# Kernel optimization log

Hardware: AMD Instinct MI355X
Metric: run time of the kernel (lower is better)

## Reference

```python
import jax, jax.numpy as jnp
import numpy as np

THRESHOLD = 2.0 / 3.0


def _quantize_1_58_bit(weight):
    """BitNet b1.58: ternary {-1,0,+1} * scale, scale = mean(|w|) clamped."""
    scale = jnp.clip(jnp.mean(jnp.abs(weight)), 1e-5, 1000.0)
    weight_norm = jnp.clip(weight / scale, -10.0, 10.0)
    q = jnp.where(weight_norm > THRESHOLD, 1.0,
                  jnp.where(weight_norm < -THRESHOLD, -1.0, 0.0)).astype(weight.dtype)
    return q, scale


def setup_inputs() -> dict:
    key = jax.random.key(0)
    k1, k2 = jax.random.split(key)
    B, S, D_IN, D_OUT = 4, 2048, 4096, 4096
    x = jax.random.normal(k1, (B, S, D_IN), dtype=jnp.float32)
    weight = jax.random.normal(k2, (D_OUT, D_IN), dtype=jnp.float32)
    bias = jnp.zeros((D_OUT,), dtype=jnp.float32)
    return {"x": x, "weight": weight, "bias": bias}


def reference(x, weight, bias):
    # Training-path forward value == eval-path forward value:
    # dequantized ternary weight, F.linear semantics (x @ W.T + b).
    q, scale = _quantize_1_58_bit(weight)
    weight_q = q * scale  # [out, in]
    out = jnp.einsum('bsi,oi->bso', x, weight_q) + bias
    return out
```

## Files before the change

kernel.cpp:

```cpp
#include <hip/hip_runtime.h>
#include <hip/hip_bf16.h>
#include <stdint.h>


typedef __bf16 bf16x8 __attribute__((ext_vector_type(8)));
typedef float f32x4 __attribute__((ext_vector_type(4)));
typedef unsigned short u16x8 __attribute__((ext_vector_type(8)));

__device__ __forceinline__ unsigned short f2bf_rne(float f) {
  union { float f; unsigned int u; } v; v.f = f;
  unsigned int u = v.u;
  u += 0x7FFFu + ((u >> 16) & 1u);
  return (unsigned short)(u >> 16);
}

__global__ void absum_kernel(const float4* __restrict__ w, int n4,
                             double* __restrict__ out) {
  float s = 0.f;
  for (int i = blockIdx.x * blockDim.x + threadIdx.x; i < n4;
       i += gridDim.x * blockDim.x) {
    float4 v = w[i];
    s += fabsf(v.x) + fabsf(v.y) + fabsf(v.z) + fabsf(v.w);
  }
#pragma unroll
  for (int off = 32; off > 0; off >>= 1) s += __shfl_down(s, off);
  __shared__ float partial[4];
  if ((threadIdx.x & 63) == 0) partial[threadIdx.x >> 6] = s;
  __syncthreads();
  if (threadIdx.x == 0)
    atomicAdd(out, (double)(partial[0] + partial[1] + partial[2] + partial[3]));
}

__global__ void quant_kernel(const float4* __restrict__ w, int n8,
                             const double* __restrict__ sum, double inv_cnt,
                             u16x8* __restrict__ q) {
  float scale = (float)fmin(fmax(sum[0] * inv_cnt, 1e-5), 1000.0);
  const float T = 2.0f / 3.0f;
  for (int i = blockIdx.x * blockDim.x + threadIdx.x; i < n8;
       i += gridDim.x * blockDim.x) {
    float4 a = w[2 * i], b = w[2 * i + 1];
    float f[8] = {a.x, a.y, a.z, a.w, b.x, b.y, b.z, b.w};
    u16x8 o;
#pragma unroll
    for (int j = 0; j < 8; ++j) {
      float n = f[j] / scale;
      o[j] = (n > T) ? 0x3F80u : ((n < -T) ? 0xBF80u : 0u);
    }
    q[i] = o;
  }
}

__global__ void xcvt_kernel(const float4* __restrict__ x, int n8,
                            u16x8* __restrict__ xb) {
  for (int i = blockIdx.x * blockDim.x + threadIdx.x; i < n8;
       i += gridDim.x * blockDim.x) {
    float4 a = x[2 * i], b = x[2 * i + 1];
    float f[8] = {a.x, a.y, a.z, a.w, b.x, b.y, b.z, b.w};
    u16x8 o;
#pragma unroll
    for (int j = 0; j < 8; ++j) o[j] = f2bf_rne(f[j]);
    xb[i] = o;
  }
}


#define BKT 64

#define FENCE() asm volatile("" ::: "memory")
#define BAR() __builtin_amdgcn_s_barrier()
#define WAIT_LGKM0() asm volatile("s_waitcnt lgkmcnt(0)" ::: "memory")
#define WAIT_VM8() asm volatile("s_waitcnt vmcnt(8)" ::: "memory")

__global__ __launch_bounds__(512, 2)
void gemm_kernel(const ushort* __restrict__ xb,
                 const ushort* __restrict__ qb,
                 const float* __restrict__ bias,
                 const double* __restrict__ sum,
                 float* __restrict__ out,
                 int M, int N, int K, double inv_cnt) {
  __shared__ __align__(16) ushort As[2][2][128][64];
  __shared__ __align__(16) ushort Bs[2][2][128][64];

  const int t = threadIdx.x;
  const int w = t >> 6;
  const int lane = t & 63;
  const int wm = w >> 2;
  const int wn = w & 3;
  const int lm = lane & 15;
  const int lk = lane >> 4;

  const int nbx = N >> 8;
  const int cpx = gridDim.x >> 3;
  const int id = blockIdx.x;
  const int swz = (id & 7) * cpx + (id >> 3);
  const int bx = swz % nbx;
  const int by = swz / nbx;
  const int m0 = by << 8;
  const int n0 = bx << 8;

  const int srow = lane >> 3;
  const int schunk = (lane & 7) ^ srow;
  const ushort* aSrc = xb + (size_t)(m0 + w * 8 + srow) * K + schunk * 8;
  const ushort* bSrc = qb + (size_t)(n0 + w * 8 + srow) * K + schunk * 8;

#define STAGE_A(BUF, H, KT)                                                    \
  do {                                                                         \
    _Pragma("unroll") for (int s_ = 0; s_ < 2; ++s_) {                         \
      __builtin_amdgcn_global_load_lds(                                        \
          (const __attribute__((address_space(1))) void*)(                     \
              aSrc + (size_t)((H) * 128 + s_ * 64) * K + (KT) * BKT),          \
          (__attribute__((address_space(3))) void*)(                           \
              &As[BUF][H][s_ * 64 + w * 8][0]),                                \
          16, 0, 0);                                                           \
    }                                                                          \
  } while (0)

#define STAGE_B(BUF, H, KT)                                                    \
  do {                                                                         \
    _Pragma("unroll") for (int s_ = 0; s_ < 2; ++s_) {                         \
      __builtin_amdgcn_global_load_lds(                                        \
          (const __attribute__((address_space(1))) void*)(                     \
              bSrc + (size_t)((H) * 128 + s_ * 64) * K + (KT) * BKT),          \
          (__attribute__((address_space(3))) void*)(                           \
              &Bs[BUF][H][s_ * 64 + w * 8][0]),                                \
          16, 0, 0);                                                           \
    }                                                                          \
  } while (0)

#define RD_A(BUF, MH)                                                          \
  _Pragma("unroll") for (int mq = 0; mq < 4; ++mq)                             \
  _Pragma("unroll") for (int ks = 0; ks < 2; ++ks)                             \
      af[mq][ks] = *(const bf16x8*)&As[BUF][wm][(MH) * 64 + mq * 16 + lm]      \
                                      [((ks * 4 + lk) ^ (lm & 7)) * 8];

#define RD_B(BUF, NF0)                                                         \
  _Pragma("unroll") for (int nf = (NF0); nf < (NF0) + 2; ++nf)                 \
  _Pragma("unroll") for (int ks = 0; ks < 2; ++ks)                             \
      bf[nf][ks] =                                                             \
          *(const bf16x8*)&Bs[BUF][wn >> 1][(wn & 1) * 64 + nf * 16 + lm]      \
                              [((ks * 4 + lk) ^ (lm & 7)) * 8];

#define MFMA_Q(MH, NB)                                                         \
  _Pragma("unroll") for (int mq = 0; mq < 4; ++mq)                             \
  _Pragma("unroll") for (int nq = 0; nq < 2; ++nq)                             \
  _Pragma("unroll") for (int ks = 0; ks < 2; ++ks)                             \
      acc[(MH) * 4 + mq][(NB) + nq] =                                          \
          __builtin_amdgcn_mfma_f32_16x16x32_bf16(                             \
              af[mq][ks], bf[(NB) + nq][ks], acc[(MH) * 4 + mq][(NB) + nq],    \
              0, 0, 0);

  f32x4 acc[8][4] = {};
  bf16x8 af[4][2];
  bf16x8 bf[4][2];

  STAGE_A(0, 0, 0); STAGE_A(0, 1, 0);
  STAGE_B(0, 0, 0); STAGE_B(0, 1, 0);
  STAGE_B(1, 0, 1); STAGE_B(1, 1, 1);
  STAGE_A(1, 0, 1); STAGE_A(1, 1, 1);
  WAIT_VM8();
  FENCE(); BAR(); FENCE();

  const int NT = K / BKT;
  for (int i = 0; i < NT / 2; ++i) {
    const int kt2 = (2 * i + 2 < NT) ? (2 * i + 2) : (NT - 1);
    const int kt3 = (2 * i + 3 < NT) ? (2 * i + 3) : (NT - 1);

    RD_A(0, 0); RD_B(0, 0);
    FENCE(); BAR(); WAIT_LGKM0();
    __builtin_amdgcn_s_setprio(1); MFMA_Q(0, 0); __builtin_amdgcn_s_setprio(0);
    FENCE(); BAR();

    RD_B(0, 2);
    FENCE(); BAR(); WAIT_LGKM0();
    __builtin_amdgcn_s_setprio(1); MFMA_Q(0, 2); __builtin_amdgcn_s_setprio(0);
    FENCE(); BAR();

    RD_A(0, 1);
    STAGE_B(0, 0, kt2); STAGE_B(0, 1, kt2);
    FENCE(); BAR(); WAIT_LGKM0();
    __builtin_amdgcn_s_setprio(1); MFMA_Q(1, 2); __builtin_amdgcn_s_setprio(0);
    FENCE(); BAR();

    STAGE_A(0, 0, kt2); STAGE_A(0, 1, kt2);
    FENCE(); BAR();
    __builtin_amdgcn_s_setprio(1); MFMA_Q(1, 0); __builtin_amdgcn_s_setprio(0);
    WAIT_VM8();
    FENCE(); BAR();

    RD_A(1, 0); RD_B(1, 0);
    FENCE(); BAR(); WAIT_LGKM0();
    __builtin_amdgcn_s_setprio(1); MFMA_Q(0, 0); __builtin_amdgcn_s_setprio(0);
    FENCE(); BAR();

    RD_B(1, 2);
    FENCE(); BAR(); WAIT_LGKM0();
    __builtin_amdgcn_s_setprio(1); MFMA_Q(0, 2); __builtin_amdgcn_s_setprio(0);
    FENCE(); BAR();

    RD_A(1, 1);
    STAGE_B(1, 0, kt3); STAGE_B(1, 1, kt3);
    FENCE(); BAR(); WAIT_LGKM0();
    __builtin_amdgcn_s_setprio(1); MFMA_Q(1, 2); __builtin_amdgcn_s_setprio(0);
    FENCE(); BAR();

    STAGE_A(1, 0, kt3); STAGE_A(1, 1, kt3);
    FENCE(); BAR();
    __builtin_amdgcn_s_setprio(1); MFMA_Q(1, 0); __builtin_amdgcn_s_setprio(0);
    WAIT_VM8();
    FENCE(); BAR();
  }

  float scale = (float)fmin(fmax(sum[0] * inv_cnt, 1e-5), 1000.0);

#pragma unroll
  for (int nf = 0; nf < 4; ++nf) {
    const int col = n0 + wn * 64 + nf * 16 + lm;
    const float bv = bias[col];
#pragma unroll
    for (int mf = 0; mf < 8; ++mf) {
      const int row = m0 + wm * 128 + mf * 16 + lk * 4;
      float* op = out + (size_t)row * N + col;
#pragma unroll
      for (int r = 0; r < 4; ++r)
        op[(size_t)r * N] = acc[mf][nf][r] * scale + bv;
    }
  }
}

extern "C" void kernel_launch(void* const* d_in, const int* in_sizes, int n_in,
                              void* d_out, int out_size, void* d_ws,
                              size_t ws_size, hipStream_t stream) {
  const float* x = (const float*)d_in[0];
  const float* w = (const float*)d_in[1];
  const float* bias = (const float*)d_in[2];
  float* out = (float*)d_out;

  const int DOUT = in_sizes[2];
  const int DIN = in_sizes[1] / DOUT;
  const int M = in_sizes[0] / DIN;
  const int N = DOUT, K = DIN;

  char* ws = (char*)d_ws;
  double* sum = (double*)ws;
  ushort* xb = (ushort*)(ws + 256);
  ushort* qb = (ushort*)(ws + 256 + (size_t)M * K * 2);

  const double inv_cnt = 1.0 / ((double)N * (double)K);

  hipMemsetAsync(d_ws, 0, 8, stream);

  const int wn4 = (N * K) / 4;
  const int wn8 = (N * K) / 8;
  absum_kernel<<<1024, 256, 0, stream>>>((const float4*)w, wn4, sum);
  quant_kernel<<<4096, 256, 0, stream>>>((const float4*)w, wn8, sum, inv_cnt,
                                         (u16x8*)qb);
  const int xn8 = (M * K) / 8;
  xcvt_kernel<<<8192, 256, 0, stream>>>((const float4*)x, xn8, (u16x8*)xb);

  const int nwg = (M >> 8) * (N >> 8);
  gemm_kernel<<<dim3(nwg), 512, 0, stream>>>(xb, qb, bias, sum, out, M, N, K,
                                             inv_cnt);
}
```

Baseline: 587.1 us.

## Replace double-buffered 256x256 GEMM with single-buffered 256x128 tiles and two-stage absum

The GEMM drops its hand-scheduled double-buffered pipeline with interleaved barriers, waitcnts and prefetch. It now uses 256x128 tiles, 256 threads, a single LDS buffer and a plain load, syncthreads, compute, syncthreads loop. The weight abs-sum reduction changes from a double atomicAdd after a memset to per-block partials plus a one-block final reduction, which removes the memset. Without overlap of global loads and MFMA, the GEMM is likely to stall on memory latency, though the smaller tiles and LDS footprint allow more resident workgroups per CU.

```diff
diff --git a/kernel.cpp b/kernel.cpp
--- a/kernel.cpp
+++ b/kernel.cpp
@@ -14,8 +14,8 @@
   return (unsigned short)(u >> 16);
 }
 
-__global__ void absum_kernel(const float4* __restrict__ w, int n4,
-                             double* __restrict__ out) {
+__global__ void absum_part(const float4* __restrict__ w, int n4,
+                           float* __restrict__ partial) {
   float s = 0.f;
   for (int i = blockIdx.x * blockDim.x + threadIdx.x; i < n4;
        i += gridDim.x * blockDim.x) {
@@ -24,11 +24,23 @@
   }
 #pragma unroll
   for (int off = 32; off > 0; off >>= 1) s += __shfl_down(s, off);
-  __shared__ float partial[4];
-  if ((threadIdx.x & 63) == 0) partial[threadIdx.x >> 6] = s;
+  __shared__ float lds[4];
+  if ((threadIdx.x & 63) == 0) lds[threadIdx.x >> 6] = s;
   __syncthreads();
   if (threadIdx.x == 0)
-    atomicAdd(out, (double)(partial[0] + partial[1] + partial[2] + partial[3]));
+    partial[blockIdx.x] = lds[0] + lds[1] + lds[2] + lds[3];
+}
+
+__global__ void absum_final(const float* __restrict__ partial, int n,
+                            double* __restrict__ out) {
+  double s = 0.0;
+  for (int i = threadIdx.x; i < n; i += blockDim.x) s += (double)partial[i];
+#pragma unroll
+  for (int off = 32; off > 0; off >>= 1) s += __shfl_down(s, off);
+  __shared__ double lds[4];
+  if ((threadIdx.x & 63) == 0) lds[threadIdx.x >> 6] = s;
+  __syncthreads();
+  if (threadIdx.x == 0) out[0] = lds[0] + lds[1] + lds[2] + lds[3];
 }
 
 __global__ void quant_kernel(const float4* __restrict__ w, int n8,
@@ -66,79 +78,49 @@
 
 #define BKT 64
 
-#define FENCE() asm volatile("" ::: "memory")
-#define BAR() __builtin_amdgcn_s_barrier()
-#define WAIT_LGKM0() asm volatile("s_waitcnt lgkmcnt(0)" ::: "memory")
-#define WAIT_VM8() asm volatile("s_waitcnt vmcnt(8)" ::: "memory")
-
-__global__ __launch_bounds__(512, 2)
+__global__ __launch_bounds__(256, 2)
 void gemm_kernel(const ushort* __restrict__ xb,
                  const ushort* __restrict__ qb,
                  const float* __restrict__ bias,
                  const double* __restrict__ sum,
                  float* __restrict__ out,
                  int M, int N, int K, double inv_cnt) {
-  __shared__ __align__(16) ushort As[2][2][128][64];
-  __shared__ __align__(16) ushort Bs[2][2][128][64];
+  __shared__ __align__(16) ushort As[256][64];
+  __shared__ __align__(16) ushort Bs[128][64];
 
   const int t = threadIdx.x;
   const int w = t >> 6;
   const int lane = t & 63;
-  const int wm = w >> 2;
-  const int wn = w & 3;
+  const int wm = w >> 1;
+  const int wn = w & 1;
   const int lm = lane & 15;
   const int lk = lane >> 4;
 
-  const int nbx = N >> 8;
+  const int nbx = N >> 7;
   const int cpx = gridDim.x >> 3;
   const int id = blockIdx.x;
   const int swz = (id & 7) * cpx + (id >> 3);
   const int bx = swz % nbx;
   const int by = swz / nbx;
   const int m0 = by << 8;
-  const int n0 = bx << 8;
+  const int n0 = bx << 7;
 
   const int srow = lane >> 3;
   const int schunk = (lane & 7) ^ srow;
   const ushort* aSrc = xb + (size_t)(m0 + w * 8 + srow) * K + schunk * 8;
   const ushort* bSrc = qb + (size_t)(n0 + w * 8 + srow) * K + schunk * 8;
 
-#define STAGE_A(BUF, H, KT)                                                    \
-  do {                                                                         \
-    _Pragma("unroll") for (int s_ = 0; s_ < 2; ++s_) {                         \
-      __builtin_amdgcn_global_load_lds(                                        \
-          (const __attribute__((address_space(1))) void*)(                     \
-              aSrc + (size_t)((H) * 128 + s_ * 64) * K + (KT) * BKT),          \
-          (__attribute__((address_space(3))) void*)(                           \
-              &As[BUF][H][s_ * 64 + w * 8][0]),                                \
-          16, 0, 0);                                                           \
-    }                                                                          \
-  } while (0)
-
-#define STAGE_B(BUF, H, KT)                                                    \
-  do {                                                                         \
-    _Pragma("unroll") for (int s_ = 0; s_ < 2; ++s_) {                         \
-      __builtin_amdgcn_global_load_lds(                                        \
-          (const __attribute__((address_space(1))) void*)(                     \
-              bSrc + (size_t)((H) * 128 + s_ * 64) * K + (KT) * BKT),          \
-          (__attribute__((address_space(3))) void*)(                           \
-              &Bs[BUF][H][s_ * 64 + w * 8][0]),                                \
-          16, 0, 0);                                                           \
-    }                                                                          \
-  } while (0)
-
-#define RD_A(BUF, MH)                                                          \
+#define RD_A(MH)                                                               \
   _Pragma("unroll") for (int mq = 0; mq < 4; ++mq)                             \
   _Pragma("unroll") for (int ks = 0; ks < 2; ++ks)                             \
-      af[mq][ks] = *(const bf16x8*)&As[BUF][wm][(MH) * 64 + mq * 16 + lm]      \
+      af[mq][ks] = *(const bf16x8*)&As[wm * 128 + (MH) * 64 + mq * 16 + lm]    \
                                       [((ks * 4 + lk) ^ (lm & 7)) * 8];
 
-#define RD_B(BUF, NF0)                                                         \
+#define RD_B(NF0)                                                              \
   _Pragma("unroll") for (int nf = (NF0); nf < (NF0) + 2; ++nf)                 \
   _Pragma("unroll") for (int ks = 0; ks < 2; ++ks)                             \
-      bf[nf][ks] =                                                             \
-          *(const bf16x8*)&Bs[BUF][wn >> 1][(wn & 1) * 64 + nf * 16 + lm]      \
-                              [((ks * 4 + lk) ^ (lm & 7)) * 8];
+      bf[nf][ks] = *(const bf16x8*)&Bs[wn * 64 + nf * 16 + lm]                 \
+                                      [((ks * 4 + lk) ^ (lm & 7)) * 8];
 
 #define MFMA_Q(MH, NB)                                                         \
   _Pragma("unroll") for (int mq = 0; mq < 4; ++mq)                             \
@@ -153,61 +135,33 @@
   bf16x8 af[4][2];
   bf16x8 bf[4][2];
 
-  STAGE_A(0, 0, 0); STAGE_A(0, 1, 0);
-  STAGE_B(0, 0, 0); STAGE_B(0, 1, 0);
-  STAGE_B(1, 0, 1); STAGE_B(1, 1, 1);
-  STAGE_A(1, 0, 1); STAGE_A(1, 1, 1);
-  WAIT_VM8();
-  FENCE(); BAR(); FENCE();
-
   const int NT = K / BKT;
-  for (int i = 0; i < NT / 2; ++i) {
-    const int kt2 = (2 * i + 2 < NT) ? (2 * i + 2) : (NT - 1);
-    const int kt3 = (2 * i + 3 < NT) ? (2 * i + 3) : (NT - 1);
-
-    RD_A(0, 0); RD_B(0, 0);
-    FENCE(); BAR(); WAIT_LGKM0();
+  for (int kt = 0; kt < NT; ++kt) {
+#pragma unroll
+    for (int s = 0; s < 8; ++s)
+      __builtin_amdgcn_global_load_lds(
+          (const __attribute__((address_space(1))) void*)(
+              aSrc + (size_t)s * 32 * K + kt * BKT),
+          (__attribute__((address_space(3))) void*)(&As[s * 32 + w * 8][0]),
+          16, 0, 0);
+#pragma unroll
+    for (int s = 0; s < 4; ++s)
+      __builtin_amdgcn_global_load_lds(
+          (const __attribute__((address_space(1))) void*)(
+              bSrc + (size_t)s * 32 * K + kt * BKT),
+          (__attribute__((address_space(3))) void*)(&Bs[s * 32 + w * 8][0]),
+          16, 0, 0);
+    __syncthreads();
+
+    RD_A(0); RD_B(0);
     __builtin_amdgcn_s_setprio(1); MFMA_Q(0, 0); __builtin_amdgcn_s_setprio(0);
-    FENCE(); BAR();
-
-    RD_B(0, 2);
-    FENCE(); BAR(); WAIT_LGKM0();
+    RD_B(2);
     __builtin_amdgcn_s_setprio(1); MFMA_Q(0, 2); __builtin_amdgcn_s_setprio(0);
-    FENCE(); BAR();
-
-    RD_A(0, 1);
-    STAGE_B(0, 0, kt2); STAGE_B(0, 1, kt2);
-    FENCE(); BAR(); WAIT_LGKM0();
+    RD_A(1);
     __builtin_amdgcn_s_setprio(1); MFMA_Q(1, 2); __builtin_amdgcn_s_setprio(0);
-    FENCE(); BAR();
-
-    STAGE_A(0, 0, kt2); STAGE_A(0, 1, kt2);
-    FENCE(); BAR();
     __builtin_amdgcn_s_setprio(1); MFMA_Q(1, 0); __builtin_amdgcn_s_setprio(0);
-    WAIT_VM8();
-    FENCE(); BAR();
-
-    RD_A(1, 0); RD_B(1, 0);
-    FENCE(); BAR(); WAIT_LGKM0();
-    __builtin_amdgcn_s_setprio(1); MFMA_Q(0, 0); __builtin_amdgcn_s_setprio(0);
-    FENCE(); BAR();
-
-    RD_B(1, 2);
-    FENCE(); BAR(); WAIT_LGKM0();
-    __builtin_amdgcn_s_setprio(1); MFMA_Q(0, 2); __builtin_amdgcn_s_setprio(0);
-    FENCE(); BAR();
-
-    RD_A(1, 1);
-    STAGE_B(1, 0, kt3); STAGE_B(1, 1, kt3);
-    FENCE(); BAR(); WAIT_LGKM0();
-    __builtin_amdgcn_s_setprio(1); MFMA_Q(1, 2); __builtin_amdgcn_s_setprio(0);
-    FENCE(); BAR();
-
-    STAGE_A(1, 0, kt3); STAGE_A(1, 1, kt3);
-    FENCE(); BAR();
-    __builtin_amdgcn_s_setprio(1); MFMA_Q(1, 0); __builtin_amdgcn_s_setprio(0);
-    WAIT_VM8();
-    FENCE(); BAR();
+
+    __syncthreads();
   }
 
   float scale = (float)fmin(fmax(sum[0] * inv_cnt, 1e-5), 1000.0);
@@ -242,22 +196,22 @@
 
   char* ws = (char*)d_ws;
   double* sum = (double*)ws;
-  ushort* xb = (ushort*)(ws + 256);
-  ushort* qb = (ushort*)(ws + 256 + (size_t)M * K * 2);
+  float* partial = (float*)(ws + 256);
+  ushort* xb = (ushort*)(ws + 4096);
+  ushort* qb = (ushort*)(ws + 4096 + (size_t)M * K * 2);
 
   const double inv_cnt = 1.0 / ((double)N * (double)K);
-
-  hipMemsetAsync(d_ws, 0, 8, stream);
 
   const int wn4 = (N * K) / 4;
   const int wn8 = (N * K) / 8;
-  absum_kernel<<<1024, 256, 0, stream>>>((const float4*)w, wn4, sum);
+  absum_part<<<256, 256, 0, stream>>>((const float4*)w, wn4, partial);
+  absum_final<<<1, 256, 0, stream>>>(partial, 256, sum);
   quant_kernel<<<4096, 256, 0, stream>>>((const float4*)w, wn8, sum, inv_cnt,
                                          (u16x8*)qb);
   const int xn8 = (M * K) / 8;
   xcvt_kernel<<<8192, 256, 0, stream>>>((const float4*)x, xn8, (u16x8*)xb);
 
-  const int nwg = (M >> 8) * (N >> 8);
-  gemm_kernel<<<dim3(nwg), 512, 0, stream>>>(xb, qb, bias, sum, out, M, N, K,
+  const int nwg = (M >> 8) * (N >> 7);
+  gemm_kernel<<<dim3(nwg), 256, 0, stream>>>(xb, qb, bias, sum, out, M, N, K,
                                              inv_cnt);
 }
```

Result: faster. 548.8 us (-6.5%).
